# Performance work log

Hardware: AMD Instinct MI355X
Metric: run time of the kernel (lower is better)

The kernel has to match this reference:

```python
import jax, jax.numpy as jnp
import numpy as np

H = 12        # num_heads
HD = 64       # head_dim
D = H * HD    # hidden_size = 768
N = 4096      # number of patches (64x64 grid)
SCALE = HD ** -0.5


def _rotate_half(x):
    half = x.shape[-1] // 2
    x1, x2 = x[..., :half], x[..., half:]
    return jnp.concatenate([-x2, x1], axis=-1)


def setup_inputs() -> dict:
    key = jax.random.key(0)
    ks = jax.random.split(key, 7)
    return {
        "hidden_states": jax.random.normal(ks[0], (N, D), jnp.float32),
        "cos": jax.random.uniform(ks[1], (N, HD), jnp.float32),
        "sin": jax.random.uniform(ks[2], (N, HD), jnp.float32),
        "qkv_w": jax.random.normal(ks[3], (D, 3 * D), jnp.float32) * (D ** -0.5),
        "qkv_b": jax.random.normal(ks[4], (3 * D,), jnp.float32) * 0.02,
        "proj_w": jax.random.normal(ks[5], (D, D), jnp.float32) * (D ** -0.5),
        "proj_b": jax.random.normal(ks[6], (D,), jnp.float32) * 0.02,
    }


def reference(hidden_states, cos, sin, qkv_w, qkv_b, proj_w, proj_b):
    n = hidden_states.shape[0]
    # fused QKV projection: (N, 3D) -> (N, 3, H, HD)
    qkv = (hidden_states @ qkv_w + qkv_b).reshape(n, 3, H, HD)
    q, k, v = qkv[:, 0], qkv[:, 1], qkv[:, 2]  # each (N, H, HD)

    # 2-D RoPE (HF apply_rotary_pos_emb_vision): cos/sin broadcast over heads
    c = cos[:, None, :]
    s = sin[:, None, :]
    q = q * c + _rotate_half(q) * s
    k = k * c + _rotate_half(k) * s

    # full bidirectional attention, heads-first layout
    q = q.transpose(1, 0, 2) * SCALE  # (H, N, HD)
    k = k.transpose(1, 0, 2)
    v = v.transpose(1, 0, 2)
    attn = jnp.einsum('hnd,hmd->hnm', q, k)      # (H, N, N)
    attn = jax.nn.softmax(attn, axis=-1)
    out = jnp.einsum('hnm,hmd->hnd', attn, v)    # (H, N, HD)
    out = out.transpose(1, 0, 2).reshape(n, D)
    return out @ proj_w + proj_b
```

## Files before the change

### kernel.cpp

```cpp
#include <hip/hip_runtime.h>
#include <stdint.h>

#define NTOK 4096
#define NH 12
#define HDIM 64
#define DMODEL 768
#define D3 2304

typedef __attribute__((ext_vector_type(8))) __bf16 bf16x8;
typedef __attribute__((ext_vector_type(4))) float f32x4;
typedef __attribute__((ext_vector_type(4))) unsigned int u32x4;

#define MFMA(a, b, c) __builtin_amdgcn_mfma_f32_16x16x32_bf16((a), (b), (c), 0, 0, 0)

__device__ __forceinline__ uint16_t f2bf(float f) {
  uint32_t u = __builtin_bit_cast(uint32_t, f) + 0x8000u;
  return (uint16_t)(u >> 16);
}
__device__ __forceinline__ uint32_t packrd(float a, float b) {
  uint32_t ua = __builtin_bit_cast(uint32_t, a) + 0x8000u;
  uint32_t ub = __builtin_bit_cast(uint32_t, b) + 0x8000u;
  return __builtin_amdgcn_perm(ub, ua, 0x07060302u);
}
__device__ __forceinline__ float bf2f(uint16_t u) {
  uint32_t v = ((uint32_t)u) << 16;
  return __builtin_bit_cast(float, v);
}
__device__ __forceinline__ void gld_lds16(const uint16_t* g, uint16_t* l) {
  __builtin_amdgcn_global_load_lds((const __attribute__((address_space(1))) void*)g,
                                   (__attribute__((address_space(3))) void*)l, 16, 0, 0);
}

__global__ void va_cast_bf16(const float* __restrict__ in, uint16_t* __restrict__ out, int n4) {
  int i = blockIdx.x * 256 + threadIdx.x;
  if (i >= n4) return;
  float4 v = ((const float4*)in)[i];
  ((uint2*)out)[i] = make_uint2(packrd(v.x, v.y), packrd(v.z, v.w));
}

__global__ void va_transpose_cast(const float* __restrict__ W, uint16_t* __restrict__ Wt,
                                  int K, int Ncols) {
  __shared__ uint16_t tile[32][36];
  const int t = threadIdx.x;
  const int k0 = blockIdx.y * 32, n0 = blockIdx.x * 32;
  {
    int i = t >> 3, j = (t & 7) * 4;
    float4 v = *(const float4*)(W + (size_t)(k0 + i) * Ncols + n0 + j);
    tile[i][j + 0] = f2bf(v.x);
    tile[i][j + 1] = f2bf(v.y);
    tile[i][j + 2] = f2bf(v.z);
    tile[i][j + 3] = f2bf(v.w);
  }
  __syncthreads();
  {
    int c = t >> 3, kk = (t & 7) * 4;
    uint32_t lo = (uint32_t)tile[kk + 0][c] | ((uint32_t)tile[kk + 1][c] << 16);
    uint32_t hi = (uint32_t)tile[kk + 2][c] | ((uint32_t)tile[kk + 3][c] << 16);
    *(uint2*)(Wt + (size_t)(n0 + c) * K + k0 + kk) = make_uint2(lo, hi);
  }
}

template <int MT, int OUT_BF16>
__global__ __launch_bounds__(256) void va_gemm64(const uint16_t* __restrict__ A,
                                                 const uint16_t* __restrict__ Bt,
                                                 const float* __restrict__ bias, void* Cout,
                                                 int M, int Nc, int K) {
  constexpr int NJ = (MT == 128) ? 4 : 2;
  __shared__ uint16_t As[2][MT * 32];
  __shared__ uint16_t Bs[2][128 * 32];
  const int t = threadIdx.x;
  const int w = t >> 6, ln = t & 63, quad = ln >> 4, l15 = ln & 15;
  const int m0 = blockIdx.y * MT, n0 = blockIdx.x * 128;
  const int wm = (MT == 128) ? (w & 1) * 64 : 0;
  const int wn = (MT == 128) ? (w >> 1) * 64 : w * 32;
  const int srow = w * 16 + (ln >> 2), schunk = (ln & 3) * 8;
  f32x4 acc[4][NJ] = {};
  for (int kk = 0; kk < K; kk += 64) {
#pragma unroll
    for (int p = 0; p < 2; ++p) {
#pragma unroll
      for (int hh = 0; hh < MT / 64; ++hh)
        gld_lds16(A + (size_t)(m0 + hh * 64 + srow) * K + kk + p * 32 + schunk,
                  &As[p][(hh * 64 + w * 16) * 32]);
#pragma unroll
      for (int hh = 0; hh < 2; ++hh)
        gld_lds16(Bt + (size_t)(n0 + hh * 64 + srow) * K + kk + p * 32 + schunk,
                  &Bs[p][(hh * 64 + w * 16) * 32]);
    }
    __syncthreads();
#pragma unroll
    for (int ko = 0; ko < 2; ++ko) {
      bf16x8 af[4], bfr[NJ];
#pragma unroll
      for (int i = 0; i < 4; ++i)
        af[i] = *(const bf16x8*)(&As[ko][(wm + i * 16 + l15) * 32 + quad * 8]);
#pragma unroll
      for (int j = 0; j < NJ; ++j)
        bfr[j] = *(const bf16x8*)(&Bs[ko][(wn + j * 16 + l15) * 32 + quad * 8]);
#pragma unroll
      for (int i = 0; i < 4; ++i)
#pragma unroll
        for (int j = 0; j < NJ; ++j) acc[i][j] = MFMA(af[i], bfr[j], acc[i][j]);
    }
    __syncthreads();
  }
#pragma unroll
  for (int i = 0; i < 4; ++i) {
    int row = m0 + wm + i * 16 + quad * 4;
#pragma unroll
    for (int j = 0; j < NJ; ++j) {
      int col = n0 + wn + j * 16 + l15;
      float b = bias[col];
      if (OUT_BF16) {
        uint16_t* C = (uint16_t*)Cout;
#pragma unroll
        for (int rg = 0; rg < 4; ++rg) C[(size_t)(row + rg) * Nc + col] = f2bf(acc[i][j][rg] + b);
      } else {
        float* C = (float*)Cout;
#pragma unroll
        for (int rg = 0; rg < 4; ++rg) C[(size_t)(row + rg) * Nc + col] = acc[i][j][rg] + b;
      }
    }
  }
}

__global__ void va_rope_split(const uint16_t* __restrict__ qkvb, const float* __restrict__ cosb,
                              const float* __restrict__ sinb, uint16_t* __restrict__ Qg,
                              uint16_t* __restrict__ Kg, uint16_t* __restrict__ Vtg) {
  const int h = blockIdx.y;
  const int lane = threadIdx.x & 63;
  const int c = threadIdx.x >> 6;
  const int n = blockIdx.x * 64 + lane;
  const uint16_t* base = qkvb + (size_t)n * D3 + h * HDIM;
  const float QS = 0.125f * 1.4426950408889634f;
  float c0[8], s0[8], c1[8], s1[8];
  *(float4*)(c0) = *(const float4*)(cosb + (size_t)n * HDIM + c * 8);
  *(float4*)(c0 + 4) = *(const float4*)(cosb + (size_t)n * HDIM + c * 8 + 4);
  *(float4*)(s0) = *(const float4*)(sinb + (size_t)n * HDIM + c * 8);
  *(float4*)(s0 + 4) = *(const float4*)(sinb + (size_t)n * HDIM + c * 8 + 4);
  *(float4*)(c1) = *(const float4*)(cosb + (size_t)n * HDIM + c * 8 + 32);
  *(float4*)(c1 + 4) = *(const float4*)(cosb + (size_t)n * HDIM + c * 8 + 36);
  *(float4*)(s1) = *(const float4*)(sinb + (size_t)n * HDIM + c * 8 + 32);
  *(float4*)(s1 + 4) = *(const float4*)(sinb + (size_t)n * HDIM + c * 8 + 36);
#pragma unroll
  for (int mtx = 0; mtx < 2; ++mtx) {
    const uint16_t* src = base + mtx * DMODEL;
    uint16_t* dst = (mtx ? Kg : Qg) + ((size_t)h * NTOK + n) * HDIM;
    const float sc = mtx ? 1.0f : QS;
    uint16_t lo[8], hi[8];
    *(uint4*)lo = *(const uint4*)(src + c * 8);
    *(uint4*)hi = *(const uint4*)(src + c * 8 + 32);
    uint32_t outlo[4], outhi[4];
#pragma unroll
    for (int j = 0; j < 8; j += 2) {
      float x0 = bf2f(lo[j]), x1 = bf2f(lo[j + 1]);
      float y0 = bf2f(hi[j]), y1 = bf2f(hi[j + 1]);
      float a0 = (x0 * c0[j] - y0 * s0[j]) * sc;
      float a1 = (x1 * c0[j + 1] - y1 * s0[j + 1]) * sc;
      float b0 = (y0 * c1[j] + x0 * s1[j]) * sc;
      float b1 = (y1 * c1[j + 1] + x1 * s1[j + 1]) * sc;
      outlo[j >> 1] = packrd(a0, a1);
      outhi[j >> 1] = packrd(b0, b1);
    }
    *(uint4*)(dst + c * 8) = *(uint4*)outlo;
    *(uint4*)(dst + c * 8 + 32) = *(uint4*)outhi;
  }
  const int H = (lane >> 4) & 1;
  const int pos = ((lane >> 2) & 3) * 8 + ((lane >> 5) & 1) * 4 + (lane & 3);
  const int col = blockIdx.x * 32 + pos;
  uint16_t vv[16];
  *(uint4*)(vv) = *(const uint4*)(base + 2 * DMODEL + c * 16);
  *(uint4*)(vv + 8) = *(const uint4*)(base + 2 * DMODEL + c * 16 + 8);
#pragma unroll
  for (int j = 0; j < 16; ++j)
    Vtg[(((size_t)H * NH + h) * HDIM + c * 16 + j) * 2048 + col] = vv[j];
}

__global__ __launch_bounds__(256, 3) void va_flash9(const uint16_t* __restrict__ Qg,
                                                    const uint16_t* __restrict__ Kg,
                                                    const uint16_t* __restrict__ Vtg,
                                                    uint16_t* __restrict__ Opb,
                                                    float* __restrict__ Lp) {
  __shared__ uint16_t Ks[2][2][64 * 32];
  __shared__ uint16_t Vs[2][2][64 * 32];
  const int t = threadIdx.x;
  const int w = t >> 6, ln = t & 63, quad = ln >> 4, l15 = ln & 15;
  const int h = blockIdx.y;
  const int qb = blockIdx.x & 31, ks = blockIdx.x >> 5;
  const int q0 = qb * 128, key0 = ks * 2048;

  bf16x8 qf[2][2];
#pragma unroll
  for (int s = 0; s < 2; ++s)
#pragma unroll
    for (int c = 0; c < 2; ++c)
      qf[s][c] = *(const bf16x8*)(Qg + ((size_t)h * NTOK + q0 + w * 32 + s * 16 + l15) * HDIM +
                                  c * 32 + quad * 8);
  const u32x4 onesu = {0x3F803F80u, 0x3F803F80u, 0x3F803F80u, 0x3F803F80u};
  const bf16x8 vones = __builtin_bit_cast(bf16x8, onesu);
  f32x4 o[2][4] = {};
  f32x4 ol[2] = {};
  const uint16_t* Kst =
      Kg + ((size_t)h * NTOK + key0 + w * 16 + (ln >> 2)) * HDIM + (ln & 3) * 8;
  const uint16_t* Vst0 =
      Vtg + (((size_t)0 * NH + h) * HDIM + w * 16 + (ln >> 2)) * 2048 + ks * 1024 + (ln & 3) * 8;
  const uint16_t* Vst1 =
      Vtg + (((size_t)1 * NH + h) * HDIM + w * 16 + (ln >> 2)) * 2048 + ks * 1024 + (ln & 3) * 8;

  gld_lds16(Kst, &Ks[0][0][w * 16 * 32]);
  gld_lds16(Kst + 32, &Ks[0][1][w * 16 * 32]);
  gld_lds16(Vst0, &Vs[0][0][w * 16 * 32]);
  gld_lds16(Vst1, &Vs[0][1][w * 16 * 32]);

  for (int kt = 0; kt < 32; ++kt) {
    __syncthreads();
    const int cur = kt & 1;
    if (kt < 31) {
      Kst += 64 * HDIM;
      Vst0 += 32;
      Vst1 += 32;
      gld_lds16(Kst, &Ks[cur ^ 1][0][w * 16 * 32]);
      gld_lds16(Kst + 32, &Ks[cur ^ 1][1][w * 16 * 32]);
      gld_lds16(Vst0, &Vs[cur ^ 1][0][w * 16 * 32]);
      gld_lds16(Vst1, &Vs[cur ^ 1][1][w * 16 * 32]);
    }
    f32x4 st[2][4];
#pragma unroll
    for (int mt = 0; mt < 4; ++mt) {
      bf16x8 ka0 = *(const bf16x8*)(&Ks[cur][0][(mt * 16 + l15) * 32 + quad * 8]);
      bf16x8 ka1 = *(const bf16x8*)(&Ks[cur][1][(mt * 16 + l15) * 32 + quad * 8]);
#pragma unroll
      for (int s = 0; s < 2; ++s) {
        f32x4 z = {};
        z = MFMA(ka0, qf[s][0], z);
        st[s][mt] = MFMA(ka1, qf[s][1], z);
      }
    }
    bf16x8 vf[4][2];
#pragma unroll
    for (int dt = 0; dt < 4; ++dt)
#pragma unroll
      for (int H = 0; H < 2; ++H)
        vf[dt][H] = *(const bf16x8*)(&Vs[cur][H][(dt * 16 + l15) * 32 + quad * 8]);
#pragma unroll
    for (int s = 0; s < 2; ++s) {
      uint32_t Ppk[4][2];
#pragma unroll
      for (int mt = 0; mt < 4; ++mt) {
        float p0 = __builtin_amdgcn_exp2f(st[s][mt][0]);
        float p1 = __builtin_amdgcn_exp2f(st[s][mt][1]);
        float p2 = __builtin_amdgcn_exp2f(st[s][mt][2]);
        float p3 = __builtin_amdgcn_exp2f(st[s][mt][3]);
        Ppk[mt][0] = packrd(p0, p1);
        Ppk[mt][1] = packrd(p2, p3);
      }
#pragma unroll
      for (int H = 0; H < 2; ++H) {
        u32x4 d = {Ppk[H][0], Ppk[H][1], Ppk[H + 2][0], Ppk[H + 2][1]};
        bf16x8 pf = __builtin_bit_cast(bf16x8, d);
#pragma unroll
        for (int dt = 0; dt < 4; ++dt) o[s][dt] = MFMA(vf[dt][H], pf, o[s][dt]);
        ol[s] = MFMA(vones, pf, ol[s]);
      }
    }
  }
  uint16_t* ob = Opb + ((size_t)(ks * NH + h) * HDIM) * NTOK;
#pragma unroll
  for (int s = 0; s < 2; ++s) {
    int q = q0 + w * 32 + s * 16 + l15;
#pragma unroll
    for (int dt = 0; dt < 4; ++dt)
#pragma unroll
      for (int rg = 0; rg < 4; ++rg)
        ob[(size_t)(dt * 16 + quad * 4 + rg) * NTOK + q] = f2bf(o[s][dt][rg]);
    if (quad == 0) Lp[(size_t)(ks * NH + h) * NTOK + q] = ol[s][0];
  }
}

__global__ __launch_bounds__(256) void va_combine2(const uint16_t* __restrict__ Opb,
                                                   const float* __restrict__ Lp,
                                                   uint16_t* __restrict__ Ob) {
  __shared__ uint16_t T[64][72];
  const int h = blockIdx.y;
  const int n0 = blockIdx.x * 64;
  const int t = threadIdx.x;
  const int lane = t & 63, c = t >> 6;
  const int n = n0 + lane;
  float lsum = Lp[(size_t)h * NTOK + n] + Lp[(size_t)(NH + h) * NTOK + n];
  const float inv = 1.0f / lsum;
#pragma unroll
  for (int j = 0; j < 16; j += 2) {
    int d = c * 16 + j;
    float r0 = 0.f, r1 = 0.f;
#pragma unroll
    for (int s = 0; s < 2; ++s) {
      const uint16_t* p = Opb + ((size_t)(s * NH + h) * HDIM + d) * NTOK + n;
      r0 += bf2f(p[0]);
      r1 += bf2f(p[NTOK]);
    }
    *(uint32_t*)(&T[lane][d]) = packrd(r0 * inv, r1 * inv);
  }
  __syncthreads();
  const int row = t >> 2, ch = t & 3;
  uint4 a = *(const uint4*)(&T[row][ch * 16]);
  uint4 b = *(const uint4*)(&T[row][ch * 16 + 8]);
  uint16_t* dst = Ob + (size_t)(n0 + row) * DMODEL + h * HDIM + ch * 16;
  *(uint4*)dst = a;
  *(uint4*)(dst + 8) = b;
}

extern "C" void kernel_launch(void* const* d_in, const int* in_sizes, int n_in, void* d_out,
                              int out_size, void* d_ws, size_t ws_size, hipStream_t stream) {
  (void)in_sizes; (void)n_in; (void)out_size; (void)ws_size;
  const float* hidden = (const float*)d_in[0];
  const float* cosb = (const float*)d_in[1];
  const float* sinb = (const float*)d_in[2];
  const float* qkv_w = (const float*)d_in[3];
  const float* qkv_b = (const float*)d_in[4];
  const float* proj_w = (const float*)d_in[5];
  const float* proj_b = (const float*)d_in[6];
  float* out = (float*)d_out;

  char* ws = (char*)d_ws;
  size_t off = 0;
  auto alloc = [&](size_t bytes) {
    void* p = ws + off;
    off += (bytes + 255) & ~(size_t)255;
    return p;
  };
  uint16_t* Abf = (uint16_t*)alloc((size_t)NTOK * DMODEL * 2);
  uint16_t* Wqt = (uint16_t*)alloc((size_t)D3 * DMODEL * 2);
  uint16_t* Wpt = (uint16_t*)alloc((size_t)DMODEL * DMODEL * 2);
  uint16_t* qkvb = (uint16_t*)alloc((size_t)NTOK * D3 * 2);
  uint16_t* Qb = (uint16_t*)alloc((size_t)NH * NTOK * HDIM * 2);
  uint16_t* Kb = (uint16_t*)alloc((size_t)NH * NTOK * HDIM * 2);
  uint16_t* Vtb = (uint16_t*)alloc((size_t)2 * NH * HDIM * 2048 * 2);
  uint16_t* Ob = (uint16_t*)alloc((size_t)NTOK * DMODEL * 2);
  uint16_t* Opb = (uint16_t*)alloc((size_t)2 * NH * HDIM * NTOK * 2);
  float* Lp = (float*)alloc((size_t)2 * NH * NTOK * 4);

  va_cast_bf16<<<(NTOK * DMODEL / 4 + 255) / 256, 256, 0, stream>>>(hidden, Abf,
                                                                    NTOK * DMODEL / 4);
  va_transpose_cast<<<dim3(D3 / 32, DMODEL / 32), 256, 0, stream>>>(qkv_w, Wqt, DMODEL, D3);
  va_transpose_cast<<<dim3(DMODEL / 32, DMODEL / 32), 256, 0, stream>>>(proj_w, Wpt, DMODEL,
                                                                        DMODEL);
  va_gemm64<128, 1><<<dim3(D3 / 128, NTOK / 128), 256, 0, stream>>>(Abf, Wqt, qkv_b, qkvb, NTOK,
                                                                    D3, DMODEL);
  va_rope_split<<<dim3(NTOK / 64, NH), 256, 0, stream>>>(qkvb, cosb, sinb, Qb, Kb, Vtb);
  va_flash9<<<dim3(64, NH), 256, 0, stream>>>(Qb, Kb, Vtb, Opb, Lp);
  va_combine2<<<dim3(NTOK / 64, NH), 256, 0, stream>>>(Opb, Lp, Ob);
  va_gemm64<64, 0><<<dim3(DMODEL / 128, NTOK / 64), 256, 0, stream>>>(Ob, Wpt, proj_b, out, NTOK,
                                                                      DMODEL, DMODEL);
}
```

Measured before the change: 211.1 us.

## Fuse RoPE and Q/K/V split into QKV GEMM epilogue, truncate P packing

```diff
diff --git a/kernel.cpp b/kernel.cpp
--- a/kernel.cpp
+++ b/kernel.cpp
@@ -21,6 +21,10 @@
   uint32_t ua = __builtin_bit_cast(uint32_t, a) + 0x8000u;
   uint32_t ub = __builtin_bit_cast(uint32_t, b) + 0x8000u;
   return __builtin_amdgcn_perm(ub, ua, 0x07060302u);
+}
+__device__ __forceinline__ uint32_t packtr(float a, float b) {
+  return __builtin_amdgcn_perm(__builtin_bit_cast(uint32_t, b), __builtin_bit_cast(uint32_t, a),
+                               0x07060302u);
 }
 __device__ __forceinline__ float bf2f(uint16_t u) {
   uint32_t v = ((uint32_t)u) << 16;
@@ -60,127 +64,135 @@
   }
 }
 
-template <int MT, int OUT_BF16>
-__global__ __launch_bounds__(256) void va_gemm64(const uint16_t* __restrict__ A,
-                                                 const uint16_t* __restrict__ Bt,
-                                                 const float* __restrict__ bias, void* Cout,
-                                                 int M, int Nc, int K) {
-  constexpr int NJ = (MT == 128) ? 4 : 2;
-  __shared__ uint16_t As[2][MT * 32];
-  __shared__ uint16_t Bs[2][128 * 32];
+__global__ __launch_bounds__(256) void va_gemm_qkv(const uint16_t* __restrict__ A,
+                                                   const uint16_t* __restrict__ Bt,
+                                                   const float* __restrict__ bias,
+                                                   const float* __restrict__ cosb,
+                                                   const float* __restrict__ sinb,
+                                                   uint16_t* __restrict__ Qg,
+                                                   uint16_t* __restrict__ Kg,
+                                                   uint16_t* __restrict__ Vtg) {
+  __shared__ uint16_t As[128 * 32];
+  __shared__ uint16_t Bs[128 * 32];
   const int t = threadIdx.x;
   const int w = t >> 6, ln = t & 63, quad = ln >> 4, l15 = ln & 15;
-  const int m0 = blockIdx.y * MT, n0 = blockIdx.x * 128;
-  const int wm = (MT == 128) ? (w & 1) * 64 : 0;
-  const int wn = (MT == 128) ? (w >> 1) * 64 : w * 32;
-  const int srow = w * 16 + (ln >> 2), schunk = (ln & 3) * 8;
-  f32x4 acc[4][NJ] = {};
-  for (int kk = 0; kk < K; kk += 64) {
+  const int m0 = blockIdx.y * 128, n0 = blockIdx.x * 128;
+  const int wm = (w & 1) * 64, wn = (w >> 1) * 64;
+  const int srow = t >> 2, scol = (t & 3) * 8;
+  f32x4 acc[4][4] = {};
+  for (int kk = 0; kk < DMODEL; kk += 32) {
 #pragma unroll
     for (int p = 0; p < 2; ++p) {
-#pragma unroll
-      for (int hh = 0; hh < MT / 64; ++hh)
-        gld_lds16(A + (size_t)(m0 + hh * 64 + srow) * K + kk + p * 32 + schunk,
-                  &As[p][(hh * 64 + w * 16) * 32]);
-#pragma unroll
-      for (int hh = 0; hh < 2; ++hh)
-        gld_lds16(Bt + (size_t)(n0 + hh * 64 + srow) * K + kk + p * 32 + schunk,
-                  &Bs[p][(hh * 64 + w * 16) * 32]);
-    }
-    __syncthreads();
-#pragma unroll
-    for (int ko = 0; ko < 2; ++ko) {
-      bf16x8 af[4], bfr[NJ];
-#pragma unroll
-      for (int i = 0; i < 4; ++i)
-        af[i] = *(const bf16x8*)(&As[ko][(wm + i * 16 + l15) * 32 + quad * 8]);
-#pragma unroll
-      for (int j = 0; j < NJ; ++j)
-        bfr[j] = *(const bf16x8*)(&Bs[ko][(wn + j * 16 + l15) * 32 + quad * 8]);
-#pragma unroll
-      for (int i = 0; i < 4; ++i)
-#pragma unroll
-        for (int j = 0; j < NJ; ++j) acc[i][j] = MFMA(af[i], bfr[j], acc[i][j]);
-    }
+      gld_lds16(A + (size_t)(m0 + p * 64 + srow) * DMODEL + kk + scol,
+                As + (p * 64 + w * 16) * 32);
+      gld_lds16(Bt + (size_t)(n0 + p * 64 + srow) * DMODEL + kk + scol,
+                Bs + (p * 64 + w * 16) * 32);
+    }
+    __syncthreads();
+    bf16x8 af[4], bfr[4];
+#pragma unroll
+    for (int i = 0; i < 4; ++i) {
+      af[i] = *(const bf16x8*)(As + (wm + i * 16 + l15) * 32 + quad * 8);
+      bfr[i] = *(const bf16x8*)(Bs + (wn + i * 16 + l15) * 32 + quad * 8);
+    }
+#pragma unroll
+    for (int i = 0; i < 4; ++i)
+#pragma unroll
+      for (int j = 0; j < 4; ++j) acc[i][j] = MFMA(af[i], bfr[j], acc[i][j]);
+    __syncthreads();
+  }
+  const int col0 = n0 + wn;
+  const int type = col0 / DMODEL;
+  const int h = (col0 % DMODEL) / HDIM;
+  if (type < 2) {
+    const float sc = (type == 0) ? (0.125f * 1.4426950408889634f) : 1.0f;
+    uint16_t* dst = (type == 0 ? Qg : Kg) + (size_t)h * NTOK * HDIM;
+#pragma unroll
+    for (int j = 0; j < 2; ++j) {
+      const int d = j * 16 + l15, dhi = d + 32;
+      const float blo = bias[col0 + d], bhi = bias[col0 + dhi];
+#pragma unroll
+      for (int i = 0; i < 4; ++i) {
+        const int row0 = m0 + wm + i * 16 + quad * 4;
+#pragma unroll
+        for (int rg = 0; rg < 4; ++rg) {
+          const int n = row0 + rg;
+          const float a = acc[i][j][rg] + blo;
+          const float b = acc[i][j + 2][rg] + bhi;
+          const float cl = cosb[(size_t)n * HDIM + d], sl = sinb[(size_t)n * HDIM + d];
+          const float ch = cosb[(size_t)n * HDIM + dhi], sh = sinb[(size_t)n * HDIM + dhi];
+          dst[(size_t)n * HDIM + d] = f2bf((a * cl - b * sl) * sc);
+          dst[(size_t)n * HDIM + dhi] = f2bf((b * ch + a * sh) * sc);
+        }
+      }
+    }
+  } else {
+    const int win = (m0 + wm) >> 6;
+#pragma unroll
+    for (int i = 0; i < 4; ++i) {
+      const int H = i & 1, hb = (i >> 1) & 1;
+      const int colp = win * 32 + quad * 8 + hb * 4;
+#pragma unroll
+      for (int j = 0; j < 4; ++j) {
+        const int d = j * 16 + l15;
+        const float bb = bias[col0 + d];
+        uint32_t u0 = packrd(acc[i][j][0] + bb, acc[i][j][1] + bb);
+        uint32_t u1 = packrd(acc[i][j][2] + bb, acc[i][j][3] + bb);
+        *(uint2*)(Vtg + (((size_t)H * NH + h) * HDIM + d) * 2048 + colp) = make_uint2(u0, u1);
+      }
+    }
+  }
+}
+
+__global__ __launch_bounds__(256) void va_gemm_proj(const uint16_t* __restrict__ A,
+                                                    const uint16_t* __restrict__ Bt,
+                                                    const float* __restrict__ bias,
+                                                    float* __restrict__ C, int M, int Nc, int K) {
+  __shared__ uint16_t As[64 * 32];
+  __shared__ uint16_t Bs[128 * 32];
+  const int t = threadIdx.x;
+  const int w = t >> 6, ln = t & 63, quad = ln >> 4, l15 = ln & 15;
+  const int m0 = blockIdx.y * 64, n0 = blockIdx.x * 128;
+  const int wn = w * 32;
+  const int srow = t >> 2, scol = (t & 3) * 8;
+  f32x4 acc[4][2] = {};
+  for (int kk = 0; kk < K; kk += 32) {
+    if (srow < 64)
+      gld_lds16(A + (size_t)(m0 + srow) * K + kk + scol, As + w * 16 * 32);
+#pragma unroll
+    for (int p = 0; p < 2; ++p)
+      gld_lds16(Bt + (size_t)(n0 + p * 64 + srow) * K + kk + scol, Bs + (p * 64 + w * 16) * 32);
+    __syncthreads();
+    bf16x8 af[4], bfr[2];
+#pragma unroll
+    for (int i = 0; i < 4; ++i) af[i] = *(const bf16x8*)(As + (i * 16 + l15) * 32 + quad * 8);
+#pragma unroll
+    for (int j = 0; j < 2; ++j)
+      bfr[j] = *(const bf16x8*)(Bs + (wn + j * 16 + l15) * 32 + quad * 8);
+#pragma unroll
+    for (int i = 0; i < 4; ++i)
+#pragma unroll
+      for (int j = 0; j < 2; ++j) acc[i][j] = MFMA(af[i], bfr[j], acc[i][j]);
     __syncthreads();
   }
 #pragma unroll
   for (int i = 0; i < 4; ++i) {
-    int row = m0 + wm + i * 16 + quad * 4;
-#pragma unroll
-    for (int j = 0; j < NJ; ++j) {
+    int row = m0 + i * 16 + quad * 4;
+#pragma unroll
+    for (int j = 0; j < 2; ++j) {
       int col = n0 + wn + j * 16 + l15;
       float b = bias[col];
-      if (OUT_BF16) {
-        uint16_t* C = (uint16_t*)Cout;
-#pragma unroll
-        for (int rg = 0; rg < 4; ++rg) C[(size_t)(row + rg) * Nc + col] = f2bf(acc[i][j][rg] + b);
-      } else {
-        float* C = (float*)Cout;
-#pragma unroll
-        for (int rg = 0; rg < 4; ++rg) C[(size_t)(row + rg) * Nc + col] = acc[i][j][rg] + b;
-      }
-    }
-  }
-}
-
-__global__ void va_rope_split(const uint16_t* __restrict__ qkvb, const float* __restrict__ cosb,
-                              const float* __restrict__ sinb, uint16_t* __restrict__ Qg,
-                              uint16_t* __restrict__ Kg, uint16_t* __restrict__ Vtg) {
-  const int h = blockIdx.y;
-  const int lane = threadIdx.x & 63;
-  const int c = threadIdx.x >> 6;
-  const int n = blockIdx.x * 64 + lane;
-  const uint16_t* base = qkvb + (size_t)n * D3 + h * HDIM;
-  const float QS = 0.125f * 1.4426950408889634f;
-  float c0[8], s0[8], c1[8], s1[8];
-  *(float4*)(c0) = *(const float4*)(cosb + (size_t)n * HDIM + c * 8);
-  *(float4*)(c0 + 4) = *(const float4*)(cosb + (size_t)n * HDIM + c * 8 + 4);
-  *(float4*)(s0) = *(const float4*)(sinb + (size_t)n * HDIM + c * 8);
-  *(float4*)(s0 + 4) = *(const float4*)(sinb + (size_t)n * HDIM + c * 8 + 4);
-  *(float4*)(c1) = *(const float4*)(cosb + (size_t)n * HDIM + c * 8 + 32);
-  *(float4*)(c1 + 4) = *(const float4*)(cosb + (size_t)n * HDIM + c * 8 + 36);
-  *(float4*)(s1) = *(const float4*)(sinb + (size_t)n * HDIM + c * 8 + 32);
-  *(float4*)(s1 + 4) = *(const float4*)(sinb + (size_t)n * HDIM + c * 8 + 36);
-#pragma unroll
-  for (int mtx = 0; mtx < 2; ++mtx) {
-    const uint16_t* src = base + mtx * DMODEL;
-    uint16_t* dst = (mtx ? Kg : Qg) + ((size_t)h * NTOK + n) * HDIM;
-    const float sc = mtx ? 1.0f : QS;
-    uint16_t lo[8], hi[8];
-    *(uint4*)lo = *(const uint4*)(src + c * 8);
-    *(uint4*)hi = *(const uint4*)(src + c * 8 + 32);
-    uint32_t outlo[4], outhi[4];
-#pragma unroll
-    for (int j = 0; j < 8; j += 2) {
-      float x0 = bf2f(lo[j]), x1 = bf2f(lo[j + 1]);
-      float y0 = bf2f(hi[j]), y1 = bf2f(hi[j + 1]);
-      float a0 = (x0 * c0[j] - y0 * s0[j]) * sc;
-      float a1 = (x1 * c0[j + 1] - y1 * s0[j + 1]) * sc;
-      float b0 = (y0 * c1[j] + x0 * s1[j]) * sc;
-      float b1 = (y1 * c1[j + 1] + x1 * s1[j + 1]) * sc;
-      outlo[j >> 1] = packrd(a0, a1);
-      outhi[j >> 1] = packrd(b0, b1);
-    }
-    *(uint4*)(dst + c * 8) = *(uint4*)outlo;
-    *(uint4*)(dst + c * 8 + 32) = *(uint4*)outhi;
-  }
-  const int H = (lane >> 4) & 1;
-  const int pos = ((lane >> 2) & 3) * 8 + ((lane >> 5) & 1) * 4 + (lane & 3);
-  const int col = blockIdx.x * 32 + pos;
-  uint16_t vv[16];
-  *(uint4*)(vv) = *(const uint4*)(base + 2 * DMODEL + c * 16);
-  *(uint4*)(vv + 8) = *(const uint4*)(base + 2 * DMODEL + c * 16 + 8);
-#pragma unroll
-  for (int j = 0; j < 16; ++j)
-    Vtg[(((size_t)H * NH + h) * HDIM + c * 16 + j) * 2048 + col] = vv[j];
-}
-
-__global__ __launch_bounds__(256, 3) void va_flash9(const uint16_t* __restrict__ Qg,
-                                                    const uint16_t* __restrict__ Kg,
-                                                    const uint16_t* __restrict__ Vtg,
-                                                    uint16_t* __restrict__ Opb,
-                                                    float* __restrict__ Lp) {
+#pragma unroll
+      for (int rg = 0; rg < 4; ++rg) C[(size_t)(row + rg) * Nc + col] = acc[i][j][rg] + b;
+    }
+  }
+}
+
+__global__ __launch_bounds__(256, 3) void va_flash10(const uint16_t* __restrict__ Qg,
+                                                     const uint16_t* __restrict__ Kg,
+                                                     const uint16_t* __restrict__ Vtg,
+                                                     uint16_t* __restrict__ Opb,
+                                                     float* __restrict__ Lp) {
   __shared__ uint16_t Ks[2][2][64 * 32];
   __shared__ uint16_t Vs[2][2][64 * 32];
   const int t = threadIdx.x;
@@ -251,8 +263,8 @@
         float p1 = __builtin_amdgcn_exp2f(st[s][mt][1]);
         float p2 = __builtin_amdgcn_exp2f(st[s][mt][2]);
         float p3 = __builtin_amdgcn_exp2f(st[s][mt][3]);
-        Ppk[mt][0] = packrd(p0, p1);
-        Ppk[mt][1] = packrd(p2, p3);
+        Ppk[mt][0] = packtr(p0, p1);
+        Ppk[mt][1] = packtr(p2, p3);
       }
 #pragma unroll
       for (int H = 0; H < 2; ++H) {
@@ -331,7 +343,6 @@
   uint16_t* Abf = (uint16_t*)alloc((size_t)NTOK * DMODEL * 2);
   uint16_t* Wqt = (uint16_t*)alloc((size_t)D3 * DMODEL * 2);
   uint16_t* Wpt = (uint16_t*)alloc((size_t)DMODEL * DMODEL * 2);
-  uint16_t* qkvb = (uint16_t*)alloc((size_t)NTOK * D3 * 2);
   uint16_t* Qb = (uint16_t*)alloc((size_t)NH * NTOK * HDIM * 2);
   uint16_t* Kb = (uint16_t*)alloc((size_t)NH * NTOK * HDIM * 2);
   uint16_t* Vtb = (uint16_t*)alloc((size_t)2 * NH * HDIM * 2048 * 2);
@@ -344,11 +355,10 @@
   va_transpose_cast<<<dim3(D3 / 32, DMODEL / 32), 256, 0, stream>>>(qkv_w, Wqt, DMODEL, D3);
   va_transpose_cast<<<dim3(DMODEL / 32, DMODEL / 32), 256, 0, stream>>>(proj_w, Wpt, DMODEL,
                                                                         DMODEL);
-  va_gemm64<128, 1><<<dim3(D3 / 128, NTOK / 128), 256, 0, stream>>>(Abf, Wqt, qkv_b, qkvb, NTOK,
-                                                                    D3, DMODEL);
-  va_rope_split<<<dim3(NTOK / 64, NH), 256, 0, stream>>>(qkvb, cosb, sinb, Qb, Kb, Vtb);
-  va_flash9<<<dim3(64, NH), 256, 0, stream>>>(Qb, Kb, Vtb, Opb, Lp);
+  va_gemm_qkv<<<dim3(D3 / 128, NTOK / 128), 256, 0, stream>>>(Abf, Wqt, qkv_b, cosb, sinb, Qb,
+                                                              Kb, Vtb);
+  va_flash10<<<dim3(64, NH), 256, 0, stream>>>(Qb, Kb, Vtb, Opb, Lp);
   va_combine2<<<dim3(NTOK / 64, NH), 256, 0, stream>>>(Opb, Lp, Ob);
-  va_gemm64<64, 0><<<dim3(DMODEL / 128, NTOK / 64), 256, 0, stream>>>(Ob, Wpt, proj_b, out, NTOK,
-                                                                      DMODEL, DMODEL);
-}
+  va_gemm_proj<<<dim3(DMODEL / 128, NTOK / 64), 256, 0, stream>>>(Ob, Wpt, proj_b, out, NTOK,
+                                                                  DMODEL, DMODEL);
+}
```

After: 200.2 us. 5.2% less time.
